# Optimization experiments

Hardware: AMD Instinct MI355X
Metric: run time of the kernel (lower is better)

## Reference

```python
import jax, jax.numpy as jnp
import numpy as np

N = 100_000      # nodes
E = 1_600_000    # edges
F_IN = 4         # num_features
H = 128          # hidden_channels
C = 5            # num_classes
G = 256          # graphs in batch


def setup_inputs() -> dict:
    key = jax.random.key(0)
    ks = jax.random.split(key, 14)
    x = jax.random.normal(ks[0], (N, F_IN), dtype=jnp.float32)
    edge_index = jax.random.randint(ks[1], (2, E), 0, N, dtype=jnp.int64)
    batch = jnp.sort(jax.random.randint(ks[2], (N,), 0, G, dtype=jnp.int64))
    def lin(k, fan_in, fan_out):
        kw, kb = jax.random.split(k)
        s = 1.0 / np.sqrt(fan_in)
        W = jax.random.uniform(kw, (fan_in, fan_out), jnp.float32, -s, s)
        b = jax.random.uniform(kb, (fan_out,), jnp.float32, -s, s)
        return W, b
    W1, b1 = lin(ks[3], F_IN, H)
    W2, b2 = lin(ks[4], H, H)
    W3, b3 = lin(ks[5], H, H)
    W4, b4 = lin(ks[6], H, H)
    Wl, bl = lin(ks[7], H, C)
    return {"x": x, "edge_index": edge_index, "batch": batch,
            "W1": W1, "b1": b1, "W2": W2, "b2": b2,
            "W3": W3, "b3": b3, "W4": W4, "b4": b4,
            "Wl": Wl, "bl": bl}


def reference(x, edge_index, batch, W1, b1, W2, b2, W3, b3, W4, b4, Wl, bl):
    n = x.shape[0]
    loop = jnp.arange(n, dtype=edge_index.dtype)
    src = jnp.concatenate([edge_index[0], loop])  # [E+N], with self-loops
    dst = jnp.concatenate([edge_index[1], loop])
    # symmetric normalization on A + I (PyG GCNConv default)
    deg = jax.ops.segment_sum(jnp.ones_like(dst, dtype=x.dtype), dst, num_segments=n)
    dinv = deg ** -0.5  # deg >= 1 thanks to self-loops
    coef = dinv[src] * dinv[dst]  # per-edge norm [E+N]

    def conv(h, W, b):
        h = h @ W                               # [N, H]
        msg = h[src] * coef[:, None]            # gather + scale [E+N, H]
        return jax.ops.segment_sum(msg, dst, num_segments=n) + b

    h = jax.nn.relu(conv(x, W1, b1))
    h = jax.nn.relu(conv(h, W2, b2))
    h = jax.nn.relu(conv(h, W3, b3))
    h = jax.nn.relu(conv(h, W4, b4))

    # global_mean_pool over graph ids
    counts = jax.ops.segment_sum(jnp.ones((n,), h.dtype), batch, num_segments=G)
    pooled = jax.ops.segment_sum(h, batch, num_segments=G)
    pooled = pooled / jnp.maximum(counts, 1.0)[:, None]  # [G, H]

    return jax.nn.sigmoid(pooled @ Wl + bl)  # [G, C]
```

## Files before the change

### kernel.cpp

```cpp
#include <hip/hip_runtime.h>
#include <hip/hip_fp8.h>
#include <math.h>

#define N_NODES 100000
#define N_EDGES 1600000
#define F_IN    4
#define HID     128
#define N_CLS   5
#define N_GRAPH 256
#define POOL_SEG 8

#define BSHIFT   9
#define BSIZE    512
#define NBUK     196
#define NCHUNK   200
#define CHUNK    8000

typedef _Float16 f16;
typedef _Float16 f16x2 __attribute__((ext_vector_type(2)));
typedef _Float16 f16x8 __attribute__((ext_vector_type(8)));
typedef float f32x4 __attribute__((ext_vector_type(4)));

__device__ __forceinline__ float rec_coef(unsigned r) {
    return (float)__builtin_bit_cast(_Float16, (unsigned short)(r & 0x7FFFu));
}

__device__ __forceinline__ float2 fp8x2_to_f32x2(unsigned short raw) {
    __hip_fp8x2_e4m3 t;
    t.__x = raw;
    return static_cast<float2>(t);
}

__device__ __forceinline__ void fma8(float c, uint2 v, float* acc) {
    float2 p0 = fp8x2_to_f32x2((unsigned short)(v.x & 0xFFFFu));
    float2 p1 = fp8x2_to_f32x2((unsigned short)(v.x >> 16));
    float2 p2 = fp8x2_to_f32x2((unsigned short)(v.y & 0xFFFFu));
    float2 p3 = fp8x2_to_f32x2((unsigned short)(v.y >> 16));
    acc[0] = fmaf(c, p0.x, acc[0]); acc[1] = fmaf(c, p0.y, acc[1]);
    acc[2] = fmaf(c, p1.x, acc[2]); acc[3] = fmaf(c, p1.y, acc[3]);
    acc[4] = fmaf(c, p2.x, acc[4]); acc[5] = fmaf(c, p2.y, acc[5]);
    acc[6] = fmaf(c, p3.x, acc[6]); acc[7] = fmaf(c, p3.y, acc[7]);
}

__global__ __launch_bounds__(256) void k_bc(const int* __restrict__ dst, int* __restrict__ C) {
    __shared__ int cnt[NBUK];
    int t = threadIdx.x;
    if (t < NBUK) cnt[t] = 0;
    __syncthreads();
    int base = blockIdx.x * CHUNK;
#pragma unroll
    for (int it = 0; it < 32; ++it) {
        int idx = it * 256 + t;
        if (idx < CHUNK) atomicAdd(&cnt[dst[base + idx] >> BSHIFT], 1);
    }
    __syncthreads();
    if (t < NBUK) C[blockIdx.x * NBUK + t] = cnt[t];
}

__global__ __launch_bounds__(256) void k_bscan(const int* __restrict__ C, int* __restrict__ Off,
                                               int* __restrict__ bbase) {
    __shared__ int s[256];
    int b = threadIdx.x;
    int tot = 0;
    if (b < NBUK) {
        for (int c = 0; c < NCHUNK; ++c) {
            Off[c * NBUK + b] = tot;
            tot += C[c * NBUK + b];
        }
    }
    s[b] = (b < NBUK) ? tot : 0;
    __syncthreads();
    for (int off = 1; off < 256; off <<= 1) {
        int v = (b >= off) ? s[b - off] : 0;
        __syncthreads();
        s[b] += v;
        __syncthreads();
    }
    if (b < NBUK) bbase[b] = s[b] - tot;
    if (b == 0) bbase[NBUK] = N_EDGES;
}

__global__ __launch_bounds__(256) void k_scatter(const int* __restrict__ src, const int* __restrict__ dst,
                                                 const int* __restrict__ Off, const int* __restrict__ bbase,
                                                 unsigned* __restrict__ bkt) {
    __shared__ int cur[NBUK];
    int t = threadIdx.x;
    if (t < NBUK) cur[t] = bbase[t] + Off[blockIdx.x * NBUK + t];
    __syncthreads();
    int base = blockIdx.x * CHUNK;
#pragma unroll
    for (int it = 0; it < 32; ++it) {
        int idx = it * 256 + t;
        if (idx < CHUNK) {
            int s = src[base + idx], d = dst[base + idx];
            int b = d >> BSHIFT;
            int p = atomicAdd(&cur[b], 1);
            bkt[p] = ((unsigned)s << BSHIFT) | (unsigned)(d & (BSIZE - 1));
        }
    }
}

__global__ __launch_bounds__(256) void k_hist2(const unsigned* __restrict__ bkt,
                                               const int* __restrict__ bbase,
                                               int* __restrict__ deg, float* __restrict__ dinv,
                                               int* __restrict__ padTot) {
    __shared__ int hist[BSIZE];
    __shared__ int tot;
    int t = threadIdx.x, b = blockIdx.x;
    hist[t] = 0; hist[t + 256] = 0;
    if (t == 0) tot = 0;
    __syncthreads();
    int s0 = bbase[b], s1 = bbase[b + 1];
    for (int e = s0 + t; e < s1; e += 256) atomicAdd(&hist[bkt[e] & (BSIZE - 1)], 1);
    __syncthreads();
    int loc = 0;
#pragma unroll
    for (int h = 0; h < 2; ++h) {
        int l = t + h * 256;
        int node = b * BSIZE + l;
        int d = hist[l];
        if (node < N_NODES) {
            deg[node] = d;
            dinv[node] = rsqrtf((float)d + 1.0f);
        }
        loc += (d + 15) >> 4;
    }
    atomicAdd(&tot, loc);
    __syncthreads();
    if (t == 0) padTot[b] = tot << 4;
}

__global__ __launch_bounds__(256) void k_pscan(const int* __restrict__ padTot, int* __restrict__ padBase,
                                               int* __restrict__ rowptrP) {
    __shared__ int s[256];
    int b = threadIdx.x;
    int v = (b < NBUK) ? padTot[b] : 0;
    s[b] = v;
    __syncthreads();
    for (int off = 1; off < 256; off <<= 1) {
        int u = (b >= off) ? s[b - off] : 0;
        __syncthreads();
        s[b] += u;
        __syncthreads();
    }
    if (b < NBUK) padBase[b] = s[b] - v;
    if (b == 0) {
        padBase[NBUK] = s[NBUK - 1];
        rowptrP[N_NODES] = s[NBUK - 1];
    }
}

__global__ __launch_bounds__(256) void k_local2(const unsigned* __restrict__ bkt,
                                                const int* __restrict__ bbase,
                                                const int* __restrict__ deg,
                                                const float* __restrict__ dinv,
                                                const int* __restrict__ padBase,
                                                int* __restrict__ rowptrP,
                                                unsigned* __restrict__ edges) {
    __shared__ int sc[BSIZE];
    __shared__ int cur[BSIZE];
    __shared__ float dv[BSIZE];
    int t = threadIdx.x, b = blockIdx.x;
    int base = padBase[b];
    int n0 = b * BSIZE + t, n1 = n0 + 256;
    int d0 = (n0 < N_NODES) ? deg[n0] : 0;
    int d1 = (n1 < N_NODES) ? deg[n1] : 0;
    int p0 = ((d0 + 15) >> 4) << 4;
    int p1 = ((d1 + 15) >> 4) << 4;
    sc[t] = p0; sc[t + 256] = p1;
    dv[t] = (n0 < N_NODES) ? dinv[n0] : 0.f;
    dv[t + 256] = (n1 < N_NODES) ? dinv[n1] : 0.f;
    __syncthreads();
    for (int off = 1; off < BSIZE; off <<= 1) {
        int i0 = t, i1 = t + 256;
        int v0 = (i0 >= off) ? sc[i0 - off] : 0;
        int v1 = (i1 >= off) ? sc[i1 - off] : 0;
        __syncthreads();
        sc[i0] += v0; sc[i1] += v1;
        __syncthreads();
    }
    int off0 = base + sc[t] - p0;
    int off1 = base + sc[t + 256] - p1;
    if (n0 < N_NODES) rowptrP[n0] = off0;
    if (n1 < N_NODES) rowptrP[n1] = off1;
    cur[t] = off0; cur[t + 256] = off1;
    int padT = sc[BSIZE - 1];
    for (int i = base + t; i < base + padT; i += 256) edges[i] = 0;
    __syncthreads();
    int s0 = bbase[b], s1 = bbase[b + 1];
    for (int e = s0 + t; e < s1; e += 256) {
        unsigned r = bkt[e];
        int dl = (int)(r & (BSIZE - 1));
        int s = (int)(r >> BSHIFT);
        int p = atomicAdd(&cur[dl], 1);
        float c = dv[dl] * dinv[s];
        unsigned short cb = __builtin_bit_cast(unsigned short, (f16)c);
        edges[p] = ((unsigned)s << 15) | (unsigned)(cb & 0x7FFFu);
    }
}

__global__ __launch_bounds__(256) void k_aggx1(const float4* __restrict__ x,
                                               const int* __restrict__ rowptrP,
                                               const unsigned* __restrict__ edges,
                                               const float* __restrict__ dinv,
                                               const float* __restrict__ W1, const float* __restrict__ b1,
                                               unsigned* __restrict__ hA) {
    __shared__ float4 sxa[16];
    __shared__ float sW[4 * HID];
    __shared__ float sb[HID];
    int t = threadIdx.x;
    sW[t] = W1[t];
    sW[t + 256] = W1[t + 256];
    if (t < HID) sb[t] = b1[t];
    int grp = t >> 4;
    int l = t & 15;
    int node = blockIdx.x * 16 + grp;
    int beg = rowptrP[node], end = rowptrP[node + 1];
    float ax = 0.f, ay = 0.f, az = 0.f, aw = 0.f;
    for (int e = beg + l; e < end; e += 16) {
        unsigned r = edges[e];
        float c = rec_coef(r);
        float4 v = x[r >> 15];
        ax = fmaf(c, v.x, ax); ay = fmaf(c, v.y, ay);
        az = fmaf(c, v.z, az); aw = fmaf(c, v.w, aw);
    }
#pragma unroll
    for (int off = 1; off < 16; off <<= 1) {
        ax += __shfl_xor(ax, off, 64);
        ay += __shfl_xor(ay, off, 64);
        az += __shfl_xor(az, off, 64);
        aw += __shfl_xor(aw, off, 64);
    }
    if (l == 0) {
        float di = dinv[node];
        float c0 = di * di;
        float4 xv = x[node];
        sxa[grp] = make_float4(fmaf(c0, xv.x, ax), fmaf(c0, xv.y, ay),
                               fmaf(c0, xv.z, az), fmaf(c0, xv.w, aw));
    }
    __syncthreads();

    int node0 = blockIdx.x * 16;
#pragma unroll
    for (int it = 0; it < 2; ++it) {
        int id = it * 256 + t;
        int n = id >> 5;
        int g = id & 31;
        float4 a = sxa[n];
        float c[4];
#pragma unroll
        for (int j = 0; j < 4; ++j) {
            int col = g * 4 + j;
            float v = sb[col];
            v = fmaf(a.x, sW[col],           v);
            v = fmaf(a.y, sW[HID + col],     v);
            v = fmaf(a.z, sW[2 * HID + col], v);
            v = fmaf(a.w, sW[3 * HID + col], v);
            c[j] = fmaxf(v, 0.0f);
        }
        unsigned lo = __hip_fp8x2_e4m3(make_float2(c[0], c[1])).__x;
        unsigned hi = __hip_fp8x2_e4m3(make_float2(c[2], c[3])).__x;
        hA[(node0 + n) * 32 + g] = lo | (hi << 16);
    }
}

template <bool FP8OUT>
__global__ __launch_bounds__(1024, 8) void k_aggemm8(const unsigned* __restrict__ h8,
                                                     const int* __restrict__ rowptrP,
                                                     const unsigned* __restrict__ edges,
                                                     const float* __restrict__ dinv,
                                                     const f16* __restrict__ Wp,
                                                     const float* __restrict__ bias,
                                                     void* __restrict__ outv) {
    __shared__ f16 S[16 * HID];
    int wave = threadIdx.x >> 6;
    int lane = threadIdx.x & 63;
    int node0 = blockIdx.x * 16;
    int node = node0 + wave;
    int g = lane >> 4;
    int l = lane & 15;
    int beg = rowptrP[node], end = rowptrP[node + 1];
    const char* hp = (const char*)h8 + l * 8;

    float acc[8];
    {
        float di = dinv[node];
        float c0 = (g == 0) ? di * di : 0.0f;
        uint2 v = *(const uint2*)(hp + ((size_t)node << 7));
        float2 p0 = fp8x2_to_f32x2((unsigned short)(v.x & 0xFFFFu));
        float2 p1 = fp8x2_to_f32x2((unsigned short)(v.x >> 16));
        float2 p2 = fp8x2_to_f32x2((unsigned short)(v.y & 0xFFFFu));
        float2 p3 = fp8x2_to_f32x2((unsigned short)(v.y >> 16));
        acc[0] = c0 * p0.x; acc[1] = c0 * p0.y;
        acc[2] = c0 * p1.x; acc[3] = c0 * p1.y;
        acc[4] = c0 * p2.x; acc[5] = c0 * p2.y;
        acc[6] = c0 * p3.x; acc[7] = c0 * p3.y;
    }

    for (int e = beg; e < end; e += 16) {
        unsigned rec16 = edges[e + l];
#pragma unroll
        for (int i = 0; i < 4; ++i) {
            unsigned rec = __shfl(rec16, i * 4 + g, 64);
            float c = rec_coef(rec);
            uint2 v = *(const uint2*)(hp + ((rec >> 8) & 0xFFFFFF80u));
            fma8(c, v, acc);
        }
    }

#pragma unroll
    for (int j = 0; j < 8; ++j) {
        acc[j] += __shfl_xor(acc[j], 16, 64);
        acc[j] += __shfl_xor(acc[j], 32, 64);
    }
    if (lane < 16) {
        f16x8 o;
#pragma unroll
        for (int j = 0; j < 8; ++j) o[j] = (f16)acc[j];
        int dw = (l * 4) ^ ((wave & 7) << 2);
        *(f16x8*)&S[wave * HID + dw * 2] = o;
    }
    __syncthreads();

    if (wave < 8) {
        int t = wave;
        int m = lane & 15;
        int q = lane >> 4;
        f32x4 c4 = (f32x4){0.f, 0.f, 0.f, 0.f};
#pragma unroll
        for (int ks = 0; ks < 4; ++ks) {
            int dw = (ks * 16 + q * 4) ^ ((m & 7) << 2);
            f16x8 a = *(const f16x8*)&S[m * HID + dw * 2];
            f16x8 b = *(const f16x8*)(Wp + ((size_t)(t * 4 + ks) * 64 + lane) * 8);
            c4 = __builtin_amdgcn_mfma_f32_16x16x32_f16(a, b, c4, 0, 0, 0);
        }
        float bb = bias[t * 16 + m];
#pragma unroll
        for (int r = 0; r < 4; ++r) {
            float val = fmaxf(c4[r] + bb, 0.0f);
            int row = node0 + q * 4 + r;
            if constexpr (FP8OUT) {
                ((__hip_fp8_e4m3*)outv)[(size_t)row * HID + t * 16 + m] = __hip_fp8_e4m3(val);
            } else {
                ((f16*)outv)[(size_t)row * HID + t * 16 + m] = (f16)val;
            }
        }
    }
}

__global__ __launch_bounds__(256) void k_packW3(const float* __restrict__ W2, const float* __restrict__ W3,
                                                const float* __restrict__ W4, f16* __restrict__ Wp) {
    int idx = blockIdx.x * 256 + threadIdx.x;
    int which = idx >> 14;
    int r = idx & 16383;
    const float* W = (which == 0) ? W2 : (which == 1) ? W3 : W4;
    int j  = r & 7;
    int L  = (r >> 3) & 63;
    int ks = (r >> 9) & 3;
    int ct = r >> 11;
    int k = ks * 32 + (L >> 4) * 8 + j;
    int n = ct * 16 + (L & 15);
    Wp[idx] = (f16)W[k * HID + n];
}

__device__ __forceinline__ int lower_bound_batch(const int* __restrict__ batch, int val) {
    int lo = 0, hi = N_NODES;
    while (lo < hi) { int m = (lo + hi) >> 1; if (batch[m] < val) lo = m + 1; else hi = m; }
    return lo;
}

__global__ __launch_bounds__(128) void k_pool1(const f16* __restrict__ h, const int* __restrict__ batch,
                                               float* __restrict__ partials) {
    int g = blockIdx.x / POOL_SEG;
    int s = blockIdx.x % POOL_SEG;
    int f = threadIdx.x;
    int beg = lower_bound_batch(batch, g);
    int end = lower_bound_batch(batch, g + 1);
    int len = end - beg;
    int sb = beg + (int)(((long long)len * s) / POOL_SEG);
    int se = beg + (int)(((long long)len * (s + 1)) / POOL_SEG);
    float acc = 0.0f;
    for (int i = sb; i < se; ++i) acc += (float)h[i * HID + f];
    partials[(size_t)blockIdx.x * HID + f] = acc;
}

__global__ __launch_bounds__(128) void k_pool2h(const float* __restrict__ partials,
                                                const int* __restrict__ batch,
                                                const float* __restrict__ Wl, const float* __restrict__ bl,
                                                float* __restrict__ out) {
    __shared__ float sp[HID];
    int g = blockIdx.x;
    int f = threadIdx.x;
    float acc = 0.0f;
#pragma unroll
    for (int s = 0; s < POOL_SEG; ++s)
        acc += partials[(size_t)(g * POOL_SEG + s) * HID + f];
    int beg = lower_bound_batch(batch, g);
    int end = lower_bound_batch(batch, g + 1);
    sp[f] = acc / fmaxf((float)(end - beg), 1.0f);
    __syncthreads();
    if (f < N_CLS) {
        float v = bl[f];
        for (int k = 0; k < HID; ++k) v = fmaf(sp[k], Wl[k * N_CLS + f], v);
        out[g * N_CLS + f] = 1.0f / (1.0f + expf(-v));
    }
}

extern "C" void kernel_launch(void* const* d_in, const int* in_sizes, int n_in,
                              void* d_out, int out_size, void* d_ws, size_t ws_size,
                              hipStream_t stream) {
    const float* x     = (const float*)d_in[0];
    const int*   ei    = (const int*)d_in[1];
    const int*   batch = (const int*)d_in[2];
    const float* W1 = (const float*)d_in[3];  const float* b1 = (const float*)d_in[4];
    const float* W2 = (const float*)d_in[5];  const float* b2 = (const float*)d_in[6];
    const float* W3 = (const float*)d_in[7];  const float* b3 = (const float*)d_in[8];
    const float* W4 = (const float*)d_in[9];  const float* b4 = (const float*)d_in[10];
    const float* Wl = (const float*)d_in[11]; const float* bl = (const float*)d_in[12];
    float* out = (float*)d_out;

    const size_t EPAD = (size_t)N_EDGES + (size_t)N_NODES * 16;

    char* p = (char*)d_ws;
    auto alloc = [&](size_t bytes) { char* r = p; p += (bytes + 255) & ~(size_t)255; return (void*)r; };
    int*      C       = (int*)     alloc((size_t)NCHUNK * NBUK * 4);
    int*      Off     = (int*)     alloc((size_t)NCHUNK * NBUK * 4);
    int*      bbase   = (int*)     alloc((size_t)(NBUK + 1) * 4);
    int*      padTot  = (int*)     alloc((size_t)NBUK * 4);
    int*      padBase = (int*)     alloc((size_t)(NBUK + 1) * 4);
    unsigned* bkt     = (unsigned*)alloc((size_t)N_EDGES * 4);
    int*      deg     = (int*)     alloc((size_t)N_NODES * 4);
    int*      rowptrP = (int*)     alloc((size_t)(N_NODES + 1) * 4);
    float*    dinv    = (float*)   alloc((size_t)N_NODES * 4);
    unsigned* edges   = (unsigned*)alloc(EPAD * 4);
    unsigned* hA      = (unsigned*)alloc((size_t)N_NODES * HID);
    unsigned* hC      = (unsigned*)alloc((size_t)N_NODES * HID);
    f16*      h4      = (f16*)     alloc((size_t)N_NODES * HID * 2);
    float*    parts   = (float*)   alloc((size_t)N_GRAPH * POOL_SEG * HID * 4);
    f16*      Wp      = (f16*)     alloc((size_t)3 * HID * HID * 2);
    f16*      Wp2 = Wp;
    f16*      Wp3 = Wp + HID * HID;
    f16*      Wp4 = Wp + 2 * HID * HID;

    const int* srcv = ei;
    const int* dstv = ei + N_EDGES;

    k_bc     <<<NCHUNK, 256, 0, stream>>>(dstv, C);
    k_bscan  <<<1, 256, 0, stream>>>(C, Off, bbase);
    k_scatter<<<NCHUNK, 256, 0, stream>>>(srcv, dstv, Off, bbase, bkt);
    k_hist2  <<<NBUK, 256, 0, stream>>>(bkt, bbase, deg, dinv, padTot);
    k_pscan  <<<1, 256, 0, stream>>>(padTot, padBase, rowptrP);
    k_local2 <<<NBUK, 256, 0, stream>>>(bkt, bbase, deg, dinv, padBase, rowptrP, edges);

    k_packW3<<<192, 256, 0, stream>>>(W2, W3, W4, Wp);

    k_aggx1<<<N_NODES / 16, 256, 0, stream>>>((const float4*)x, rowptrP, edges, dinv, W1, b1, hA);

    const int fgrid = N_NODES / 16;
    k_aggemm8<true ><<<fgrid, 1024, 0, stream>>>(hA, rowptrP, edges, dinv, Wp2, b2, hC);
    k_aggemm8<true ><<<fgrid, 1024, 0, stream>>>(hC, rowptrP, edges, dinv, Wp3, b3, hA);
    k_aggemm8<false><<<fgrid, 1024, 0, stream>>>(hA, rowptrP, edges, dinv, Wp4, b4, h4);

    k_pool1 <<<N_GRAPH * POOL_SEG, 128, 0, stream>>>(h4, batch, parts);
    k_pool2h<<<N_GRAPH, 128, 0, stream>>>(parts, batch, Wl, bl, out);
}
```

Measured before the change: 357.6 us.

## Group nodes by padded degree bin so blocks process similar-degree nodes

```diff
diff --git a/kernel.cpp b/kernel.cpp
--- a/kernel.cpp
+++ b/kernel.cpp
@@ -15,6 +15,7 @@
 #define NBUK     196
 #define NCHUNK   200
 #define CHUNK    8000
+#define NBIN     8
 
 typedef _Float16 f16;
 typedef _Float16 f16x2 __attribute__((ext_vector_type(2)));
@@ -103,12 +104,14 @@
 __global__ __launch_bounds__(256) void k_hist2(const unsigned* __restrict__ bkt,
                                                const int* __restrict__ bbase,
                                                int* __restrict__ deg, float* __restrict__ dinv,
-                                               int* __restrict__ padTot) {
+                                               int* __restrict__ padTot, int* __restrict__ binCnt) {
     __shared__ int hist[BSIZE];
     __shared__ int tot;
+    __shared__ int bc[NBIN];
     int t = threadIdx.x, b = blockIdx.x;
     hist[t] = 0; hist[t + 256] = 0;
     if (t == 0) tot = 0;
+    if (t < NBIN) bc[t] = 0;
     __syncthreads();
     int s0 = bbase[b], s1 = bbase[b + 1];
     for (int e = s0 + t; e < s1; e += 256) atomicAdd(&hist[bkt[e] & (BSIZE - 1)], 1);
@@ -122,17 +125,23 @@
         if (node < N_NODES) {
             deg[node] = d;
             dinv[node] = rsqrtf((float)d + 1.0f);
-        }
-        loc += (d + 15) >> 4;
+            int bin = (d + 15) >> 4;
+            if (bin > NBIN - 1) bin = NBIN - 1;
+            atomicAdd(&bc[bin], 1);
+            loc += (d + 15) >> 4;
+        }
     }
     atomicAdd(&tot, loc);
     __syncthreads();
     if (t == 0) padTot[b] = tot << 4;
+    if (t < NBIN) binCnt[t * NBUK + b] = bc[t];
 }
 
 __global__ __launch_bounds__(256) void k_pscan(const int* __restrict__ padTot, int* __restrict__ padBase,
-                                               int* __restrict__ rowptrP) {
+                                               int* __restrict__ rowptrP,
+                                               const int* __restrict__ binCnt, int* __restrict__ binOff) {
     __shared__ int s[256];
+    __shared__ int s2[256];
     int b = threadIdx.x;
     int v = (b < NBUK) ? padTot[b] : 0;
     s[b] = v;
@@ -147,6 +156,48 @@
     if (b == 0) {
         padBase[NBUK] = s[NBUK - 1];
         rowptrP[N_NODES] = s[NBUK - 1];
+    }
+    int loc[7];
+    int sum = 0;
+    int base = b * 7;
+#pragma unroll
+    for (int j = 0; j < 7; ++j) {
+        int idx = base + j;
+        int u = (idx < NBIN * NBUK) ? binCnt[idx] : 0;
+        loc[j] = sum; sum += u;
+    }
+    s2[b] = sum;
+    __syncthreads();
+    for (int off = 1; off < 256; off <<= 1) {
+        int u = (b >= off) ? s2[b - off] : 0;
+        __syncthreads();
+        s2[b] += u;
+        __syncthreads();
+    }
+    int excl = s2[b] - sum;
+#pragma unroll
+    for (int j = 0; j < 7; ++j) {
+        int idx = base + j;
+        if (idx < NBIN * NBUK) binOff[idx] = excl + loc[j];
+    }
+}
+
+__global__ __launch_bounds__(256) void k_order(const int* __restrict__ deg,
+                                               const int* __restrict__ binOff,
+                                               int* __restrict__ order) {
+    __shared__ int cur[NBIN];
+    int t = threadIdx.x, b = blockIdx.x;
+    if (t < NBIN) cur[t] = binOff[t * NBUK + b];
+    __syncthreads();
+#pragma unroll
+    for (int h = 0; h < 2; ++h) {
+        int node = b * BSIZE + t + h * 256;
+        if (node < N_NODES) {
+            int bin = (deg[node] + 15) >> 4;
+            if (bin > NBIN - 1) bin = NBIN - 1;
+            int p = atomicAdd(&cur[bin], 1);
+            order[p] = node;
+        }
     }
 }
 
@@ -203,9 +254,11 @@
                                                const int* __restrict__ rowptrP,
                                                const unsigned* __restrict__ edges,
                                                const float* __restrict__ dinv,
+                                               const int* __restrict__ order,
                                                const float* __restrict__ W1, const float* __restrict__ b1,
                                                unsigned* __restrict__ hA) {
     __shared__ float4 sxa[16];
+    __shared__ int sni[16];
     __shared__ float sW[4 * HID];
     __shared__ float sb[HID];
     int t = threadIdx.x;
@@ -214,7 +267,7 @@
     if (t < HID) sb[t] = b1[t];
     int grp = t >> 4;
     int l = t & 15;
-    int node = blockIdx.x * 16 + grp;
+    int node = order[blockIdx.x * 16 + grp];
     int beg = rowptrP[node], end = rowptrP[node + 1];
     float ax = 0.f, ay = 0.f, az = 0.f, aw = 0.f;
     for (int e = beg + l; e < end; e += 16) {
@@ -237,10 +290,10 @@
         float4 xv = x[node];
         sxa[grp] = make_float4(fmaf(c0, xv.x, ax), fmaf(c0, xv.y, ay),
                                fmaf(c0, xv.z, az), fmaf(c0, xv.w, aw));
-    }
-    __syncthreads();
-
-    int node0 = blockIdx.x * 16;
+        sni[grp] = node;
+    }
+    __syncthreads();
+
 #pragma unroll
     for (int it = 0; it < 2; ++it) {
         int id = it * 256 + t;
@@ -260,7 +313,7 @@
         }
         unsigned lo = __hip_fp8x2_e4m3(make_float2(c[0], c[1])).__x;
         unsigned hi = __hip_fp8x2_e4m3(make_float2(c[2], c[3])).__x;
-        hA[(node0 + n) * 32 + g] = lo | (hi << 16);
+        hA[sni[n] * 32 + g] = lo | (hi << 16);
     }
 }
 
@@ -269,18 +322,22 @@
                                                      const int* __restrict__ rowptrP,
                                                      const unsigned* __restrict__ edges,
                                                      const float* __restrict__ dinv,
+                                                     const int* __restrict__ order,
                                                      const f16* __restrict__ Wp,
                                                      const float* __restrict__ bias,
                                                      void* __restrict__ outv) {
     __shared__ f16 S[16 * HID];
+    __shared__ int sn[16];
     int wave = threadIdx.x >> 6;
     int lane = threadIdx.x & 63;
     int node0 = blockIdx.x * 16;
-    int node = node0 + wave;
+    int node = order[node0 + wave];
     int g = lane >> 4;
     int l = lane & 15;
     int beg = rowptrP[node], end = rowptrP[node + 1];
     const char* hp = (const char*)h8 + l * 8;
+
+    if (lane == 0) sn[wave] = node;
 
     float acc[8];
     {
@@ -338,7 +395,7 @@
 #pragma unroll
         for (int r = 0; r < 4; ++r) {
             float val = fmaxf(c4[r] + bb, 0.0f);
-            int row = node0 + q * 4 + r;
+            int row = sn[q * 4 + r];
             if constexpr (FP8OUT) {
                 ((__hip_fp8_e4m3*)outv)[(size_t)row * HID + t * 16 + m] = __hip_fp8_e4m3(val);
             } else {
@@ -428,6 +485,9 @@
     int*      bbase   = (int*)     alloc((size_t)(NBUK + 1) * 4);
     int*      padTot  = (int*)     alloc((size_t)NBUK * 4);
     int*      padBase = (int*)     alloc((size_t)(NBUK + 1) * 4);
+    int*      binCnt  = (int*)     alloc((size_t)NBIN * NBUK * 4);
+    int*      binOff  = (int*)     alloc((size_t)NBIN * NBUK * 4);
+    int*      order   = (int*)     alloc((size_t)N_NODES * 4);
     unsigned* bkt     = (unsigned*)alloc((size_t)N_EDGES * 4);
     int*      deg     = (int*)     alloc((size_t)N_NODES * 4);
     int*      rowptrP = (int*)     alloc((size_t)(N_NODES + 1) * 4);
@@ -448,18 +508,19 @@
     k_bc     <<<NCHUNK, 256, 0, stream>>>(dstv, C);
     k_bscan  <<<1, 256, 0, stream>>>(C, Off, bbase);
     k_scatter<<<NCHUNK, 256, 0, stream>>>(srcv, dstv, Off, bbase, bkt);
-    k_hist2  <<<NBUK, 256, 0, stream>>>(bkt, bbase, deg, dinv, padTot);
-    k_pscan  <<<1, 256, 0, stream>>>(padTot, padBase, rowptrP);
+    k_hist2  <<<NBUK, 256, 0, stream>>>(bkt, bbase, deg, dinv, padTot, binCnt);
+    k_pscan  <<<1, 256, 0, stream>>>(padTot, padBase, rowptrP, binCnt, binOff);
+    k_order  <<<NBUK, 256, 0, stream>>>(deg, binOff, order);
     k_local2 <<<NBUK, 256, 0, stream>>>(bkt, bbase, deg, dinv, padBase, rowptrP, edges);
 
     k_packW3<<<192, 256, 0, stream>>>(W2, W3, W4, Wp);
 
-    k_aggx1<<<N_NODES / 16, 256, 0, stream>>>((const float4*)x, rowptrP, edges, dinv, W1, b1, hA);
+    k_aggx1<<<N_NODES / 16, 256, 0, stream>>>((const float4*)x, rowptrP, edges, dinv, order, W1, b1, hA);
 
     const int fgrid = N_NODES / 16;
-    k_aggemm8<true ><<<fgrid, 1024, 0, stream>>>(hA, rowptrP, edges, dinv, Wp2, b2, hC);
-    k_aggemm8<true ><<<fgrid, 1024, 0, stream>>>(hC, rowptrP, edges, dinv, Wp3, b3, hA);
-    k_aggemm8<false><<<fgrid, 1024, 0, stream>>>(hA, rowptrP, edges, dinv, Wp4, b4, h4);
+    k_aggemm8<true ><<<fgrid, 1024, 0, stream>>>(hA, rowptrP, edges, dinv, order, Wp2, b2, hC);
+    k_aggemm8<true ><<<fgrid, 1024, 0, stream>>>(hC, rowptrP, edges, dinv, order, Wp3, b3, hA);
+    k_aggemm8<false><<<fgrid, 1024, 0, stream>>>(hA, rowptrP, edges, dinv, order, Wp4, b4, h4);
 
     k_pool1 <<<N_GRAPH * POOL_SEG, 128, 0, stream>>>(h4, batch, parts);
     k_pool2h<<<N_GRAPH, 128, 0, stream>>>(parts, batch, Wl, bl, out);
```

After: 368.8 us. 1.03x slower.

## Fuse CSR build kernels with fixed per-bucket padding and fold weight packing

Applied to the files above, without the earlier changes.

```diff
diff --git a/kernel.cpp b/kernel.cpp
--- a/kernel.cpp
+++ b/kernel.cpp
@@ -15,6 +15,7 @@
 #define NBUK     196
 #define NCHUNK   200
 #define CHUNK    8000
+#define BUKPAD   8192
 
 typedef _Float16 f16;
 typedef _Float16 f16x2 __attribute__((ext_vector_type(2)));
@@ -42,19 +43,35 @@
     acc[6] = fmaf(c, p3.x, acc[6]); acc[7] = fmaf(c, p3.y, acc[7]);
 }
 
-__global__ __launch_bounds__(256) void k_bc(const int* __restrict__ dst, int* __restrict__ C) {
-    __shared__ int cnt[NBUK];
+__global__ __launch_bounds__(256) void k_bcp(const int* __restrict__ dst, int* __restrict__ C,
+                                             const float* __restrict__ W2, const float* __restrict__ W3,
+                                             const float* __restrict__ W4, f16* __restrict__ Wp) {
     int t = threadIdx.x;
-    if (t < NBUK) cnt[t] = 0;
-    __syncthreads();
-    int base = blockIdx.x * CHUNK;
-#pragma unroll
-    for (int it = 0; it < 32; ++it) {
-        int idx = it * 256 + t;
-        if (idx < CHUNK) atomicAdd(&cnt[dst[base + idx] >> BSHIFT], 1);
-    }
-    __syncthreads();
-    if (t < NBUK) C[blockIdx.x * NBUK + t] = cnt[t];
+    if (blockIdx.x < NCHUNK) {
+        __shared__ int cnt[NBUK];
+        if (t < NBUK) cnt[t] = 0;
+        __syncthreads();
+        int base = blockIdx.x * CHUNK;
+#pragma unroll
+        for (int it = 0; it < 32; ++it) {
+            int idx = it * 256 + t;
+            if (idx < CHUNK) atomicAdd(&cnt[dst[base + idx] >> BSHIFT], 1);
+        }
+        __syncthreads();
+        if (t < NBUK) C[blockIdx.x * NBUK + t] = cnt[t];
+    } else {
+        int idx = (blockIdx.x - NCHUNK) * 256 + t;
+        int which = idx >> 14;
+        int r = idx & 16383;
+        const float* W = (which == 0) ? W2 : (which == 1) ? W3 : W4;
+        int j  = r & 7;
+        int L  = (r >> 3) & 63;
+        int ks = (r >> 9) & 3;
+        int ct = r >> 11;
+        int k = ks * 32 + (L >> 4) * 8 + j;
+        int n = ct * 16 + (L & 15);
+        Wp[idx] = (f16)W[k * HID + n];
+    }
 }
 
 __global__ __launch_bounds__(256) void k_bscan(const int* __restrict__ C, int* __restrict__ Off,
@@ -100,76 +117,20 @@
     }
 }
 
-__global__ __launch_bounds__(256) void k_hist2(const unsigned* __restrict__ bkt,
-                                               const int* __restrict__ bbase,
-                                               int* __restrict__ deg, float* __restrict__ dinv,
-                                               int* __restrict__ padTot) {
-    __shared__ int hist[BSIZE];
-    __shared__ int tot;
+__global__ __launch_bounds__(256) void k_build1(const unsigned* __restrict__ bkt,
+                                                const int* __restrict__ bbase,
+                                                int* __restrict__ deg, float* __restrict__ dinv,
+                                                int* __restrict__ rowptrP) {
+    __shared__ int hist[BSIZE], sc[BSIZE];
     int t = threadIdx.x, b = blockIdx.x;
+    int s0 = bbase[b], s1 = bbase[b + 1];
     hist[t] = 0; hist[t + 256] = 0;
-    if (t == 0) tot = 0;
-    __syncthreads();
-    int s0 = bbase[b], s1 = bbase[b + 1];
+    __syncthreads();
     for (int e = s0 + t; e < s1; e += 256) atomicAdd(&hist[bkt[e] & (BSIZE - 1)], 1);
     __syncthreads();
-    int loc = 0;
-#pragma unroll
-    for (int h = 0; h < 2; ++h) {
-        int l = t + h * 256;
-        int node = b * BSIZE + l;
-        int d = hist[l];
-        if (node < N_NODES) {
-            deg[node] = d;
-            dinv[node] = rsqrtf((float)d + 1.0f);
-        }
-        loc += (d + 15) >> 4;
-    }
-    atomicAdd(&tot, loc);
-    __syncthreads();
-    if (t == 0) padTot[b] = tot << 4;
-}
-
-__global__ __launch_bounds__(256) void k_pscan(const int* __restrict__ padTot, int* __restrict__ padBase,
-                                               int* __restrict__ rowptrP) {
-    __shared__ int s[256];
-    int b = threadIdx.x;
-    int v = (b < NBUK) ? padTot[b] : 0;
-    s[b] = v;
-    __syncthreads();
-    for (int off = 1; off < 256; off <<= 1) {
-        int u = (b >= off) ? s[b - off] : 0;
-        __syncthreads();
-        s[b] += u;
-        __syncthreads();
-    }
-    if (b < NBUK) padBase[b] = s[b] - v;
-    if (b == 0) {
-        padBase[NBUK] = s[NBUK - 1];
-        rowptrP[N_NODES] = s[NBUK - 1];
-    }
-}
-
-__global__ __launch_bounds__(256) void k_local2(const unsigned* __restrict__ bkt,
-                                                const int* __restrict__ bbase,
-                                                const int* __restrict__ deg,
-                                                const float* __restrict__ dinv,
-                                                const int* __restrict__ padBase,
-                                                int* __restrict__ rowptrP,
-                                                unsigned* __restrict__ edges) {
-    __shared__ int sc[BSIZE];
-    __shared__ int cur[BSIZE];
-    __shared__ float dv[BSIZE];
-    int t = threadIdx.x, b = blockIdx.x;
-    int base = padBase[b];
-    int n0 = b * BSIZE + t, n1 = n0 + 256;
-    int d0 = (n0 < N_NODES) ? deg[n0] : 0;
-    int d1 = (n1 < N_NODES) ? deg[n1] : 0;
-    int p0 = ((d0 + 15) >> 4) << 4;
-    int p1 = ((d1 + 15) >> 4) << 4;
+    int p0 = ((hist[t] + 15) >> 4) << 4;
+    int p1 = ((hist[t + 256] + 15) >> 4) << 4;
     sc[t] = p0; sc[t + 256] = p1;
-    dv[t] = (n0 < N_NODES) ? dinv[n0] : 0.f;
-    dv[t + 256] = (n1 < N_NODES) ? dinv[n1] : 0.f;
     __syncthreads();
     for (int off = 1; off < BSIZE; off <<= 1) {
         int i0 = t, i1 = t + 256;
@@ -179,15 +140,43 @@
         sc[i0] += v0; sc[i1] += v1;
         __syncthreads();
     }
-    int off0 = base + sc[t] - p0;
-    int off1 = base + sc[t + 256] - p1;
-    if (n0 < N_NODES) rowptrP[n0] = off0;
-    if (n1 < N_NODES) rowptrP[n1] = off1;
-    cur[t] = off0; cur[t + 256] = off1;
-    int padT = sc[BSIZE - 1];
-    for (int i = base + t; i < base + padT; i += 256) edges[i] = 0;
-    __syncthreads();
+    int base = s0 + b * BUKPAD;
+    int n0 = b * BSIZE + t, n1 = n0 + 256;
+    if (n0 < N_NODES) {
+        deg[n0] = hist[t];
+        dinv[n0] = rsqrtf((float)hist[t] + 1.0f);
+        rowptrP[n0] = base + sc[t] - p0;
+    }
+    if (n1 < N_NODES) {
+        deg[n1] = hist[t + 256];
+        dinv[n1] = rsqrtf((float)hist[t + 256] + 1.0f);
+        rowptrP[n1] = base + sc[t + 256] - p1;
+    }
+}
+
+__global__ __launch_bounds__(256) void k_fill2(const unsigned* __restrict__ bkt,
+                                               const int* __restrict__ bbase,
+                                               const int* __restrict__ deg,
+                                               const float* __restrict__ dinv,
+                                               const int* __restrict__ rowptrP,
+                                               unsigned* __restrict__ edges) {
+    __shared__ int cur[BSIZE];
+    __shared__ float dv[BSIZE];
+    int t = threadIdx.x, b = blockIdx.x;
     int s0 = bbase[b], s1 = bbase[b + 1];
+    int n0 = b * BSIZE + t, n1 = n0 + 256;
+    int d0 = (n0 < N_NODES) ? deg[n0] : 0;
+    int d1 = (n1 < N_NODES) ? deg[n1] : 0;
+    int r0 = (n0 < N_NODES) ? rowptrP[n0] : 0;
+    int r1 = (n1 < N_NODES) ? rowptrP[n1] : 0;
+    dv[t] = (n0 < N_NODES) ? dinv[n0] : 0.f;
+    dv[t + 256] = (n1 < N_NODES) ? dinv[n1] : 0.f;
+    cur[t] = r0; cur[t + 256] = r1;
+    int p0 = ((d0 + 15) >> 4) << 4;
+    int p1 = ((d1 + 15) >> 4) << 4;
+    for (int i = d0; i < p0; ++i) edges[r0 + i] = 0;
+    for (int i = d1; i < p1; ++i) edges[r1 + i] = 0;
+    __syncthreads();
     for (int e = s0 + t; e < s1; e += 256) {
         unsigned r = bkt[e];
         int dl = (int)(r & (BSIZE - 1));
@@ -201,6 +190,7 @@
 
 __global__ __launch_bounds__(256) void k_aggx1(const float4* __restrict__ x,
                                                const int* __restrict__ rowptrP,
+                                               const int* __restrict__ deg,
                                                const unsigned* __restrict__ edges,
                                                const float* __restrict__ dinv,
                                                const float* __restrict__ W1, const float* __restrict__ b1,
@@ -215,7 +205,8 @@
     int grp = t >> 4;
     int l = t & 15;
     int node = blockIdx.x * 16 + grp;
-    int beg = rowptrP[node], end = rowptrP[node + 1];
+    int beg = rowptrP[node];
+    int end = beg + (((deg[node] + 15) >> 4) << 4);
     float ax = 0.f, ay = 0.f, az = 0.f, aw = 0.f;
     for (int e = beg + l; e < end; e += 16) {
         unsigned r = edges[e];
@@ -264,14 +255,14 @@
     }
 }
 
-template <bool FP8OUT>
 __global__ __launch_bounds__(1024, 8) void k_aggemm8(const unsigned* __restrict__ h8,
                                                      const int* __restrict__ rowptrP,
+                                                     const int* __restrict__ deg,
                                                      const unsigned* __restrict__ edges,
                                                      const float* __restrict__ dinv,
                                                      const f16* __restrict__ Wp,
                                                      const float* __restrict__ bias,
-                                                     void* __restrict__ outv) {
+                                                     unsigned char* __restrict__ out8) {
     __shared__ f16 S[16 * HID];
     int wave = threadIdx.x >> 6;
     int lane = threadIdx.x & 63;
@@ -279,7 +270,8 @@
     int node = node0 + wave;
     int g = lane >> 4;
     int l = lane & 15;
-    int beg = rowptrP[node], end = rowptrP[node + 1];
+    int beg = rowptrP[node];
+    int end = beg + (((deg[node] + 15) >> 4) << 4);
     const char* hp = (const char*)h8 + l * 8;
 
     float acc[8];
@@ -339,28 +331,10 @@
         for (int r = 0; r < 4; ++r) {
             float val = fmaxf(c4[r] + bb, 0.0f);
             int row = node0 + q * 4 + r;
-            if constexpr (FP8OUT) {
-                ((__hip_fp8_e4m3*)outv)[(size_t)row * HID + t * 16 + m] = __hip_fp8_e4m3(val);
-            } else {
-                ((f16*)outv)[(size_t)row * HID + t * 16 + m] = (f16)val;
-            }
-        }
-    }
-}
-
-__global__ __launch_bounds__(256) void k_packW3(const float* __restrict__ W2, const float* __restrict__ W3,
-                                                const float* __restrict__ W4, f16* __restrict__ Wp) {
-    int idx = blockIdx.x * 256 + threadIdx.x;
-    int which = idx >> 14;
-    int r = idx & 16383;
-    const float* W = (which == 0) ? W2 : (which == 1) ? W3 : W4;
-    int j  = r & 7;
-    int L  = (r >> 3) & 63;
-    int ks = (r >> 9) & 3;
-    int ct = r >> 11;
-    int k = ks * 32 + (L >> 4) * 8 + j;
-    int n = ct * 16 + (L & 15);
-    Wp[idx] = (f16)W[k * HID + n];
+            out8[(size_t)row * HID + t * 16 + m] =
+                ((__hip_fp8_e4m3)val).__x;
+        }
+    }
 }
 
 __device__ __forceinline__ int lower_bound_batch(const int* __restrict__ batch, int val) {
@@ -369,7 +343,8 @@
     return lo;
 }
 
-__global__ __launch_bounds__(128) void k_pool1(const f16* __restrict__ h, const int* __restrict__ batch,
+__global__ __launch_bounds__(128) void k_pool1(const unsigned char* __restrict__ h8,
+                                               const int* __restrict__ batch,
                                                float* __restrict__ partials) {
     int g = blockIdx.x / POOL_SEG;
     int s = blockIdx.x % POOL_SEG;
@@ -380,7 +355,11 @@
     int sb = beg + (int)(((long long)len * s) / POOL_SEG);
     int se = beg + (int)(((long long)len * (s + 1)) / POOL_SEG);
     float acc = 0.0f;
-    for (int i = sb; i < se; ++i) acc += (float)h[i * HID + f];
+    for (int i = sb; i < se; ++i) {
+        __hip_fp8_e4m3 v;
+        v.__x = h8[(size_t)i * HID + f];
+        acc += (float)v;
+    }
     partials[(size_t)blockIdx.x * HID + f] = acc;
 }
 
@@ -419,15 +398,13 @@
     const float* Wl = (const float*)d_in[11]; const float* bl = (const float*)d_in[12];
     float* out = (float*)d_out;
 
-    const size_t EPAD = (size_t)N_EDGES + (size_t)N_NODES * 16;
+    const size_t EPAD = (size_t)N_EDGES + (size_t)NBUK * BUKPAD;
 
     char* p = (char*)d_ws;
     auto alloc = [&](size_t bytes) { char* r = p; p += (bytes + 255) & ~(size_t)255; return (void*)r; };
     int*      C       = (int*)     alloc((size_t)NCHUNK * NBUK * 4);
     int*      Off     = (int*)     alloc((size_t)NCHUNK * NBUK * 4);
     int*      bbase   = (int*)     alloc((size_t)(NBUK + 1) * 4);
-    int*      padTot  = (int*)     alloc((size_t)NBUK * 4);
-    int*      padBase = (int*)     alloc((size_t)(NBUK + 1) * 4);
     unsigned* bkt     = (unsigned*)alloc((size_t)N_EDGES * 4);
     int*      deg     = (int*)     alloc((size_t)N_NODES * 4);
     int*      rowptrP = (int*)     alloc((size_t)(N_NODES + 1) * 4);
@@ -435,7 +412,6 @@
     unsigned* edges   = (unsigned*)alloc(EPAD * 4);
     unsigned* hA      = (unsigned*)alloc((size_t)N_NODES * HID);
     unsigned* hC      = (unsigned*)alloc((size_t)N_NODES * HID);
-    f16*      h4      = (f16*)     alloc((size_t)N_NODES * HID * 2);
     float*    parts   = (float*)   alloc((size_t)N_GRAPH * POOL_SEG * HID * 4);
     f16*      Wp      = (f16*)     alloc((size_t)3 * HID * HID * 2);
     f16*      Wp2 = Wp;
@@ -445,22 +421,19 @@
     const int* srcv = ei;
     const int* dstv = ei + N_EDGES;
 
-    k_bc     <<<NCHUNK, 256, 0, stream>>>(dstv, C);
+    k_bcp    <<<NCHUNK + 192, 256, 0, stream>>>(dstv, C, W2, W3, W4, Wp);
     k_bscan  <<<1, 256, 0, stream>>>(C, Off, bbase);
     k_scatter<<<NCHUNK, 256, 0, stream>>>(srcv, dstv, Off, bbase, bkt);
-    k_hist2  <<<NBUK, 256, 0, stream>>>(bkt, bbase, deg, dinv, padTot);
-    k_pscan  <<<1, 256, 0, stream>>>(padTot, padBase, rowptrP);
-    k_local2 <<<NBUK, 256, 0, stream>>>(bkt, bbase, deg, dinv, padBase, rowptrP, edges);
-
-    k_packW3<<<192, 256, 0, stream>>>(W2, W3, W4, Wp);
-
-    k_aggx1<<<N_NODES / 16, 256, 0, stream>>>((const float4*)x, rowptrP, edges, dinv, W1, b1, hA);
+    k_build1 <<<NBUK, 256, 0, stream>>>(bkt, bbase, deg, dinv, rowptrP);
+    k_fill2  <<<NBUK, 256, 0, stream>>>(bkt, bbase, deg, dinv, rowptrP, edges);
+
+    k_aggx1<<<N_NODES / 16, 256, 0, stream>>>((const float4*)x, rowptrP, deg, edges, dinv, W1, b1, hA);
 
     const int fgrid = N_NODES / 16;
-    k_aggemm8<true ><<<fgrid, 1024, 0, stream>>>(hA, rowptrP, edges, dinv, Wp2, b2, hC);
-    k_aggemm8<true ><<<fgrid, 1024, 0, stream>>>(hC, rowptrP, edges, dinv, Wp3, b3, hA);
-    k_aggemm8<false><<<fgrid, 1024, 0, stream>>>(hA, rowptrP, edges, dinv, Wp4, b4, h4);
-
-    k_pool1 <<<N_GRAPH * POOL_SEG, 128, 0, stream>>>(h4, batch, parts);
+    k_aggemm8<<<fgrid, 1024, 0, stream>>>(hA, rowptrP, deg, edges, dinv, Wp2, b2, (unsigned char*)hC);
+    k_aggemm8<<<fgrid, 1024, 0, stream>>>(hC, rowptrP, deg, edges, dinv, Wp3, b3, (unsigned char*)hA);
+    k_aggemm8<<<fgrid, 1024, 0, stream>>>(hA, rowptrP, deg, edges, dinv, Wp4, b4, (unsigned char*)hC);
+
+    k_pool1 <<<N_GRAPH * POOL_SEG, 128, 0, stream>>>((const unsigned char*)hC, batch, parts);
     k_pool2h<<<N_GRAPH, 128, 0, stream>>>(parts, batch, Wl, bl, out);
 }
```

Measured after the change: 362.6 us. About the same (+1.4%).
